# Kernel optimization log

Measured on AMD Instinct MI355X. Metric: run time of the kernel, lower is better.

The kernel has to match this reference:

```python
import jax, jax.numpy as jnp
import numpy as np

DIM = 512
HEADS = 8
EPS = 1e-3  # keras LayerNormalization default epsilon


def setup_inputs() -> dict:
    key = jax.random.key(0)
    ks = jax.random.split(key, 12)
    B, H, W, C = 8, 32, 32, DIM
    s = 0.02
    return {
        "x": jax.random.normal(ks[0], (B, H, W, C), jnp.float32),
        "ln_gamma": jnp.ones((C,), jnp.float32),
        "ln_beta": jnp.zeros((C,), jnp.float32),
        "qkv_d_w": jax.random.normal(ks[1], (C, 3 * C), jnp.float32) * s,
        "qkv_d_b": jnp.zeros((3 * C,), jnp.float32),
        "qkv_s_w": jax.random.normal(ks[2], (C, 3 * C), jnp.float32) * s,
        "qkv_s_b": jnp.zeros((3 * C,), jnp.float32),
        "proj_d_w": jax.random.normal(ks[3], (C, C), jnp.float32) * s,
        "proj_d_b": jnp.zeros((C,), jnp.float32),
        "proj_s_w": jax.random.normal(ks[4], (C, C), jnp.float32) * s,
        "proj_s_b": jnp.zeros((C,), jnp.float32),
        "fusion_weight": jnp.ones((2,), jnp.float32),
    }


def _split_heads(t, B, N):
    # [B, N, C] -> [B, heads, N, head_dim]
    return t.reshape(B, N, HEADS, -1).transpose(0, 2, 1, 3)


def _merge_heads(t, B, N, C):
    # [B, heads, N, head_dim] -> [B, N, C]
    return t.transpose(0, 2, 1, 3).reshape(B, N, C)


def reference(x, ln_gamma, ln_beta, qkv_d_w, qkv_d_b, qkv_s_w, qkv_s_b,
              proj_d_w, proj_d_b, proj_s_w, proj_s_b, fusion_weight):
    B, H, W, C = x.shape
    N = H * W
    scale = (C // HEADS) ** -0.5

    xf = x.reshape(B, N, C)
    mu = jnp.mean(xf, axis=-1, keepdims=True)
    var = jnp.var(xf, axis=-1, keepdims=True)
    xf = (xf - mu) * jax.lax.rsqrt(var + EPS) * ln_gamma + ln_beta

    # dense (softmax) branch
    qkv_d = xf @ qkv_d_w + qkv_d_b
    q_d, k_d, v_d = (
        _split_heads(t, B, N) for t in jnp.split(qkv_d, 3, axis=-1)
    )
    logits_d = jnp.einsum("bhnd,bhmd->bhnm", q_d, k_d) * scale
    out_d = jnp.einsum("bhnm,bhmd->bhnd", jax.nn.softmax(logits_d, axis=-1), v_d)
    out_d = _merge_heads(out_d, B, N, C) @ proj_d_w + proj_d_b

    # sparse (relu^2) branch
    qkv_s = xf @ qkv_s_w + qkv_s_b
    q_s, k_s, v_s = (
        _split_heads(t, B, N) for t in jnp.split(qkv_s, 3, axis=-1)
    )
    rq = jnp.square(jax.nn.relu(q_s))
    rk = jnp.square(jax.nn.relu(k_s))
    logits_s = jnp.einsum("bhnd,bhmd->bhnm", rq, rk) * scale
    out_s = jnp.einsum("bhnm,bhmd->bhnd", logits_s, v_s)
    out_s = _merge_heads(out_s, B, N, C) @ proj_s_w + proj_s_b

    alpha = jax.nn.softmax(fusion_weight)
    out = alpha[0] * out_s + alpha[1] * out_d
    return out.reshape(B, H, W, C)
```

## Files before the change

kernel.cpp:

```cpp
#include <hip/hip_runtime.h>
#include <math.h>

#define M_ROWS   8192
#define CDIM     512
#define QKV_N    1536
#define NTOK     1024
#define HEADS    8
#define HD       64
#define EPS      1e-3f
#define SCALE    0.125f
#define SCL2E    0.18033688011112042f

typedef __attribute__((ext_vector_type(8))) short short8;
typedef __attribute__((ext_vector_type(4))) float f32x4;
typedef unsigned short ushort_t;


__device__ __forceinline__ ushort_t f2bf(float f) {
    union { float f; unsigned int u; } v; v.f = f;
    unsigned int r = v.u + 0x7fffu + ((v.u >> 16) & 1u);
    return (ushort_t)(r >> 16);
}
__device__ __forceinline__ float bf2f(ushort_t u) {
    union { unsigned int u; float f; } v; v.u = ((unsigned int)u) << 16;
    return v.f;
}

__device__ __forceinline__ void get_alpha(const float* __restrict__ fw,
                                          float& a0, float& a1)
{
    const float m  = fmaxf(fw[0], fw[1]);
    const float e0 = __expf(fw[0] - m);
    const float e1 = __expf(fw[1] - m);
    const float inv = 1.0f / (e0 + e1);
    a0 = e0 * inv;
    a1 = e1 * inv;
}


__global__ __launch_bounds__(256) void ln_kernel(const float* __restrict__ x,
                                                 const float* __restrict__ gamma,
                                                 const float* __restrict__ beta,
                                                 ushort_t* __restrict__ xhi,
                                                 ushort_t* __restrict__ xlo)
{
    const int row = blockIdx.x;
    const int t   = threadIdx.x;
    const float2 v = ((const float2*)(x + (size_t)row * CDIM))[t];
    float s  = v.x + v.y;
    float ss = v.x * v.x + v.y * v.y;
#pragma unroll
    for (int off = 32; off > 0; off >>= 1) {
        s  += __shfl_xor(s,  off, 64);
        ss += __shfl_xor(ss, off, 64);
    }
    __shared__ float red[8];
    __shared__ float stats[2];
    const int wid = t >> 6, lane = t & 63;
    if (lane == 0) { red[wid] = s; red[4 + wid] = ss; }
    __syncthreads();
    if (t == 0) {
        const float S  = red[0] + red[1] + red[2] + red[3];
        const float SS = red[4] + red[5] + red[6] + red[7];
        const float mu  = S * (1.0f / CDIM);
        const float var = SS * (1.0f / CDIM) - mu * mu;
        stats[0] = mu;
        stats[1] = rsqrtf(var + EPS);
    }
    __syncthreads();
    const float mu = stats[0], rs = stats[1];
    const float2 gv = ((const float2*)gamma)[t];
    const float2 bv = ((const float2*)beta)[t];
    const float ox = (v.x - mu) * rs * gv.x + bv.x;
    const float oy = (v.y - mu) * rs * gv.y + bv.y;
    ushort2 h2, l2;
    h2.x = f2bf(ox); l2.x = f2bf(ox - bf2f(h2.x));
    h2.y = f2bf(oy); l2.y = f2bf(oy - bf2f(h2.y));
    ((ushort2*)(xhi + (size_t)row * CDIM))[t] = h2;
    ((ushort2*)(xlo + (size_t)row * CDIM))[t] = l2;
}


__global__ __launch_bounds__(256) void tconv_kernel(const float* __restrict__ W,
                                                    ushort_t* __restrict__ hiT,
                                                    ushort_t* __restrict__ loT,
                                                    int N, int ors, int coff)
{
    const int t  = threadIdx.x;
    const int bk = blockIdx.x * 64, bn = blockIdx.y * 64;
    __shared__ float tile[64][65];
#pragma unroll
    for (int i = 0; i < 4; ++i) {
        const int idx = t + i * 256;
        const int kl = idx >> 4, nl = (idx & 15) * 4;
        const float4 v = *(const float4*)(W + (size_t)(bk + kl) * N + bn + nl);
        tile[kl][nl] = v.x; tile[kl][nl + 1] = v.y;
        tile[kl][nl + 2] = v.z; tile[kl][nl + 3] = v.w;
    }
    __syncthreads();
#pragma unroll
    for (int i = 0; i < 2; ++i) {
        const int idx = t + i * 256;
        const int nl = idx >> 3, kc = (idx & 7) * 8;
        short8 hv, lv;
#pragma unroll
        for (int j = 0; j < 8; ++j) {
            const float f = tile[kc + j][nl];
            const ushort_t h = f2bf(f);
            hv[j] = (short)h;
            lv[j] = (short)f2bf(f - bf2f(h));
        }
        const size_t ob = (size_t)(bn + nl) * ors + coff + bk + kc;
        *(short8*)(hiT + ob) = hv;
        if (loT) *(short8*)(loT + ob) = lv;
    }
}


template<int SPLIT, int OUTBF>
__global__ __launch_bounds__(256) void gemm_bf16_mfma(const ushort_t* __restrict__ Ahi,
                                                      const ushort_t* __restrict__ Alo,
                                                      const ushort_t* __restrict__ Bhi,
                                                      const ushort_t* __restrict__ Blo,
                                                      const float* __restrict__ bias,
                                                      float* __restrict__ C,
                                                      ushort_t* __restrict__ Cb,
                                                      int N, int K)
{
    const int t  = threadIdx.x;
    const int l  = t & 63, w = t >> 6;
    const int wr = w >> 1, wc = w & 1;
    const int lr = l & 15, lg = l >> 4;
    const int bm = blockIdx.x * 128, bn = blockIdx.y * 128;

    __shared__ ushort_t As[SPLIT ? 2 : 1][128 * 64];
    __shared__ ushort_t Bs[SPLIT ? 2 : 1][128 * 64];

    f32x4 acc[4][4];
#pragma unroll
    for (int i = 0; i < 4; ++i)
#pragma unroll
        for (int j = 0; j < 4; ++j) acc[i][j] = (f32x4){0.f, 0.f, 0.f, 0.f};

    const int srow0  = t >> 3;
    const int schunk = t & 7;

    for (int kt = 0; kt < K; kt += 64) {
        __syncthreads();
#pragma unroll
        for (int i = 0; i < 4; ++i) {
            const int row = srow0 + i * 32;
            const int cs  = ((schunk ^ (row & 7)) * 8);
            const size_t ga = (size_t)(bm + row) * K + kt + schunk * 8;
            const size_t gb = (size_t)(bn + row) * K + kt + schunk * 8;
            *(short8*)(&As[0][row * 64 + cs]) = *(const short8*)(Ahi + ga);
            *(short8*)(&Bs[0][row * 64 + cs]) = *(const short8*)(Bhi + gb);
            if (SPLIT) {
                *(short8*)(&As[1][row * 64 + cs]) = *(const short8*)(Alo + ga);
                *(short8*)(&Bs[1][row * 64 + cs]) = *(const short8*)(Blo + gb);
            }
        }
        __syncthreads();
#pragma unroll
        for (int ks = 0; ks < 2; ++ks) {
            short8 ah[4], bh[4], al[4], bl[4];
#pragma unroll
            for (int mf = 0; mf < 4; ++mf) {
                const int row = wr * 64 + mf * 16 + lr;
                const int cs  = (((ks * 4 + lg) ^ (row & 7)) * 8);
                ah[mf] = *(const short8*)(&As[0][row * 64 + cs]);
                if (SPLIT) al[mf] = *(const short8*)(&As[1][row * 64 + cs]);
            }
#pragma unroll
            for (int nf = 0; nf < 4; ++nf) {
                const int row = wc * 64 + nf * 16 + lr;
                const int cs  = (((ks * 4 + lg) ^ (row & 7)) * 8);
                bh[nf] = *(const short8*)(&Bs[0][row * 64 + cs]);
                if (SPLIT) bl[nf] = *(const short8*)(&Bs[1][row * 64 + cs]);
            }
#pragma unroll
            for (int mf = 0; mf < 4; ++mf)
#pragma unroll
                for (int nf = 0; nf < 4; ++nf) {
                    acc[mf][nf] = __builtin_amdgcn_mfma_f32_16x16x32_bf16(ah[mf], bh[nf], acc[mf][nf], 0, 0, 0);
                    if (SPLIT) {
                        acc[mf][nf] = __builtin_amdgcn_mfma_f32_16x16x32_bf16(al[mf], bh[nf], acc[mf][nf], 0, 0, 0);
                        acc[mf][nf] = __builtin_amdgcn_mfma_f32_16x16x32_bf16(ah[mf], bl[nf], acc[mf][nf], 0, 0, 0);
                    }
                }
        }
    }
    float bv[4];
#pragma unroll
    for (int nf = 0; nf < 4; ++nf) bv[nf] = bias[bn + wc * 64 + nf * 16 + lr];
#pragma unroll
    for (int mf = 0; mf < 4; ++mf)
#pragma unroll
        for (int r = 0; r < 4; ++r) {
            const int row = bm + wr * 64 + mf * 16 + lg * 4 + r;
            if (OUTBF) {
                ushort_t* cp = Cb + (size_t)row * N + bn + wc * 64;
#pragma unroll
                for (int nf = 0; nf < 4; ++nf)
                    cp[nf * 16 + lr] = f2bf(acc[mf][nf][r] + bv[nf]);
            } else {
                float* cp = C + (size_t)row * N + bn + wc * 64;
#pragma unroll
                for (int nf = 0; nf < 4; ++nf)
                    cp[nf * 16 + lr] = acc[mf][nf][r] + bv[nf];
            }
        }
}


__global__ __launch_bounds__(256) void vt_kernel(const ushort_t* __restrict__ qkvd_bf,
                                                 ushort_t* __restrict__ vtg)
{
    const int t  = threadIdx.x;
    const int bh = blockIdx.x, nt = blockIdx.y;
    const int b  = bh >> 3, h = bh & 7;
    __shared__ ushort_t tile[64 * 72];
    const int row = t >> 2, c16 = (t & 3) * 16;
    const size_t src = (size_t)(b * NTOK + nt * 64 + row) * QKV_N + 2 * CDIM + h * HD + c16;
    *(short8*)(tile + row * 72 + c16)     = *(const short8*)(qkvd_bf + src);
    *(short8*)(tile + row * 72 + c16 + 8) = *(const short8*)(qkvd_bf + src + 8);
    __syncthreads();
    const int d = t >> 2, tc = (t & 3) * 16;
    short8 o0, o1;
#pragma unroll
    for (int i = 0; i < 8; ++i) {
        o0[i] = (short)tile[(tc + i) * 72 + d];
        o1[i] = (short)tile[(tc + 8 + i) * 72 + d];
    }
    const size_t dst = ((size_t)bh * 64 + d) * NTOK + nt * 64 + tc;
    *(short8*)(vtg + dst)     = o0;
    *(short8*)(vtg + dst + 8) = o1;
}


__global__ __launch_bounds__(256) void attn_dense_mfma(const ushort_t* __restrict__ qkvd_bf,
                                                       const ushort_t* __restrict__ vtg,
                                                       const float* __restrict__ fw,
                                                       ushort_t* __restrict__ athi,
                                                       ushort_t* __restrict__ atlo)
{
    const int t  = threadIdx.x;
    const int l  = t & 63;
    const int w  = t >> 6;
    const int lr = l & 15;
    const int lg = l >> 4;

    const int blk = blockIdx.x;
    const int xcd = blk & 7;
    const int ixl = blk >> 3;
    const int bh  = ((ixl >> 4) << 3) + xcd;
    const int qt  = ixl & 15;
    const int b   = bh >> 3, h = bh & 7;

    __shared__ ushort_t Qs[64 * 72];
    __shared__ ushort_t Ks[64 * 72];
    __shared__ ushort_t Vs[64 * 72];
    __shared__ ushort_t Pq[64 * 72];

    const int srow = t >> 2, sc = (t & 3) * 16;

    {
        const size_t src = (size_t)(b * NTOK + qt * 64 + srow) * QKV_N + h * HD + sc;
        *(short8*)(Qs + srow * 72 + sc)     = *(const short8*)(qkvd_bf + src);
        *(short8*)(Qs + srow * 72 + sc + 8) = *(const short8*)(qkvd_bf + src + 8);
    }
    __syncthreads();

    const short8 bQ0 = *(const short8*)(Qs + (w * 16 + lr) * 72 + lg * 8);
    const short8 bQ1 = *(const short8*)(Qs + (w * 16 + lr) * 72 + 32 + lg * 8);

    f32x4 oacc[4];
#pragma unroll
    for (int i = 0; i < 4; ++i) oacc[i] = (f32x4){0.f, 0.f, 0.f, 0.f};
    float lsum = 0.f;

    for (int kt2 = 0; kt2 < 16; ++kt2) {
        __syncthreads();
        {
            const size_t ksrc = (size_t)(b * NTOK + kt2 * 64 + srow) * QKV_N + CDIM + h * HD + sc;
            *(short8*)(Ks + srow * 72 + sc)     = *(const short8*)(qkvd_bf + ksrc);
            *(short8*)(Ks + srow * 72 + sc + 8) = *(const short8*)(qkvd_bf + ksrc + 8);
            const size_t vsrc = ((size_t)bh * 64 + srow) * NTOK + kt2 * 64 + sc;
            *(short8*)(Vs + srow * 72 + sc)     = *(const short8*)(vtg + vsrc);
            *(short8*)(Vs + srow * 72 + sc + 8) = *(const short8*)(vtg + vsrc + 8);
        }
        __syncthreads();

#pragma unroll
        for (int kb = 0; kb < 4; ++kb) {
            const short8 aK0 = *(const short8*)(Ks + (kb * 16 + lr) * 72 + lg * 8);
            const short8 aK1 = *(const short8*)(Ks + (kb * 16 + lr) * 72 + 32 + lg * 8);
            f32x4 z = {0.f, 0.f, 0.f, 0.f};
            z = __builtin_amdgcn_mfma_f32_16x16x32_bf16(aK0, bQ0, z, 0, 0, 0);
            z = __builtin_amdgcn_mfma_f32_16x16x32_bf16(aK1, bQ1, z, 0, 0, 0);
            const float p0 = exp2f(z[0] * SCL2E);
            const float p1 = exp2f(z[1] * SCL2E);
            const float p2 = exp2f(z[2] * SCL2E);
            const float p3 = exp2f(z[3] * SCL2E);
            lsum += (p0 + p1) + (p2 + p3);
            unsigned int r01, r23;
            asm("v_cvt_pk_bf16_f32 %0, %1, %2" : "=v"(r01) : "v"(p0), "v"(p1));
            asm("v_cvt_pk_bf16_f32 %0, %1, %2" : "=v"(r23) : "v"(p2), "v"(p3));
            uint2 pw; pw.x = r01; pw.y = r23;
            *(uint2*)(Pq + (w * 16 + lr) * 72 + kb * 16 + lg * 4) = pw;
        }

        const short8 bP0 = *(const short8*)(Pq + (w * 16 + lr) * 72 + lg * 8);
        const short8 bP1 = *(const short8*)(Pq + (w * 16 + lr) * 72 + 32 + lg * 8);
#pragma unroll
        for (int nfd = 0; nfd < 4; ++nfd) {
            const short8 aV0 = *(const short8*)(Vs + (nfd * 16 + lr) * 72 + lg * 8);
            const short8 aV1 = *(const short8*)(Vs + (nfd * 16 + lr) * 72 + 32 + lg * 8);
            oacc[nfd] = __builtin_amdgcn_mfma_f32_16x16x32_bf16(aV0, bP0, oacc[nfd], 0, 0, 0);
            oacc[nfd] = __builtin_amdgcn_mfma_f32_16x16x32_bf16(aV1, bP1, oacc[nfd], 0, 0, 0);
        }
    }

    lsum += __shfl_xor(lsum, 16, 64);
    lsum += __shfl_xor(lsum, 32, 64);
    float a0, a1;
    get_alpha(fw, a0, a1);
    const float sc2 = a1 / lsum;
    const size_t orow = ((size_t)(b * NTOK + qt * 64 + w * 16 + lr)) * 1024 + CDIM + h * HD;
#pragma unroll
    for (int nfd = 0; nfd < 4; ++nfd) {
        ushort4 hw, lw;
#pragma unroll
        for (int r = 0; r < 4; ++r) {
            const float v = oacc[nfd][r] * sc2;
            const ushort_t hv = f2bf(v);
            ((ushort_t*)&hw)[r] = hv;
            ((ushort_t*)&lw)[r] = f2bf(v - bf2f(hv));
        }
        *(ushort4*)(athi + orow + nfd * 16 + lg * 4) = hw;
        *(ushort4*)(atlo + orow + nfd * 16 + lg * 4) = lw;
    }
}


__global__ __launch_bounds__(256) void sparse_kv_kernel(const float* __restrict__ qkvs,
                                                        float* __restrict__ kvpart)
{
    const int t     = threadIdx.x;
    const int bh    = blockIdx.x >> 2;
    const int chunk = blockIdx.x & 3;
    const int b     = bh >> 3, h = bh & 7;
    const int j     = t >> 2, g = t & 3;
    __shared__ __align__(16) float ks[64 * 68];
    __shared__ __align__(16) float vs[64 * 68];
    float4 acc[4];
#pragma unroll
    for (int c4 = 0; c4 < 4; ++c4) acc[c4] = make_float4(0.f, 0.f, 0.f, 0.f);

    const size_t bbase = (size_t)b * NTOK * QKV_N;
    for (int mt = chunk * 4; mt < chunk * 4 + 4; ++mt) {
        __syncthreads();
        {
            const float* ksrc = qkvs + bbase + (size_t)(mt * 64) * QKV_N + CDIM + h * HD;
            const float* vsrc = ksrc + CDIM;
#pragma unroll
            for (int i = 0; i < 4; ++i) {
                const int idx = t + i * 256;
                const int row = idx >> 4, c4 = (idx & 15) * 4;
                *(float4*)(ks + row * 68 + c4) = *(const float4*)(ksrc + (size_t)row * QKV_N + c4);
                *(float4*)(vs + row * 68 + c4) = *(const float4*)(vsrc + (size_t)row * QKV_N + c4);
            }
        }
        __syncthreads();
#pragma unroll 4
        for (int m = 0; m < 64; ++m) {
            const float kkv = ks[m * 68 + j];
            const float rk  = fmaxf(kkv, 0.f);
            const float rk2 = rk * rk;
#pragma unroll
            for (int c4 = 0; c4 < 4; ++c4) {
                const float4 vv = *(const float4*)(vs + m * 68 + g * 16 + c4 * 4);
                acc[c4].x += rk2 * vv.x; acc[c4].y += rk2 * vv.y;
                acc[c4].z += rk2 * vv.z; acc[c4].w += rk2 * vv.w;
            }
        }
    }
#pragma unroll
    for (int c4 = 0; c4 < 4; ++c4) {
        float4 w = acc[c4];
        w.x *= SCALE; w.y *= SCALE; w.z *= SCALE; w.w *= SCALE;
        *(float4*)(kvpart + ((size_t)blockIdx.x << 12) + j * 64 + g * 16 + c4 * 4) = w;
    }
}


__global__ __launch_bounds__(256) void sparse_out_kernel(const float* __restrict__ qkvs,
                                                         const float* __restrict__ kvpart,
                                                         const float* __restrict__ fw,
                                                         ushort_t* __restrict__ athi,
                                                         ushort_t* __restrict__ atlo)
{
    const int t   = threadIdx.x;
    const int blk = blockIdx.x;
    const int qt  = blk & 15;
    const int bh  = blk >> 4;
    const int b   = bh >> 3, h = bh & 7;
    const int r   = t >> 2, g = t & 3;
    __shared__ __align__(16) float qs[64 * 68];
    __shared__ __align__(16) float kvs[64 * 68];
    {
        const float* qsrc = qkvs + (size_t)b * NTOK * QKV_N + (size_t)(qt * 64) * QKV_N + h * HD;
        const float* p0 = kvpart + ((size_t)(bh * 4) << 12);
#pragma unroll
        for (int i = 0; i < 4; ++i) {
            const int idx = t + i * 256;
            const int row = idx >> 4, c4 = (idx & 15) * 4;
            *(float4*)(qs + row * 68 + c4) = *(const float4*)(qsrc + (size_t)row * QKV_N + c4);
            const int o = row * 64 + c4;
            float4 s0 = *(const float4*)(p0 + o);
            const float4 s1 = *(const float4*)(p0 + 4096 + o);
            const float4 s2 = *(const float4*)(p0 + 8192 + o);
            const float4 s3 = *(const float4*)(p0 + 12288 + o);
            s0.x += s1.x + s2.x + s3.x; s0.y += s1.y + s2.y + s3.y;
            s0.z += s1.z + s2.z + s3.z; s0.w += s1.w + s2.w + s3.w;
            *(float4*)(kvs + row * 68 + c4) = s0;
        }
    }
    __syncthreads();
    float4 acc[4];
#pragma unroll
    for (int c4 = 0; c4 < 4; ++c4) acc[c4] = make_float4(0.f, 0.f, 0.f, 0.f);
#pragma unroll 4
    for (int jj = 0; jj < 64; ++jj) {
        const float qv  = qs[r * 68 + jj];
        const float rq  = fmaxf(qv, 0.f);
        const float rq2 = rq * rq;
#pragma unroll
        for (int c4 = 0; c4 < 4; ++c4) {
            const float4 kvv = *(const float4*)(kvs + jj * 68 + g * 16 + c4 * 4);
            acc[c4].x += rq2 * kvv.x; acc[c4].y += rq2 * kvv.y;
            acc[c4].z += rq2 * kvv.z; acc[c4].w += rq2 * kvv.w;
        }
    }
    float a0, a1;
    get_alpha(fw, a0, a1);
    const size_t orow = ((size_t)(b * NTOK + qt * 64 + r)) * 1024 + h * HD;
#pragma unroll
    for (int c4 = 0; c4 < 4; ++c4) {
        float4 w = acc[c4];
        w.x *= a0; w.y *= a0; w.z *= a0; w.w *= a0;
        ushort4 hw, lw;
        hw.x = f2bf(w.x); lw.x = f2bf(w.x - bf2f(hw.x));
        hw.y = f2bf(w.y); lw.y = f2bf(w.y - bf2f(hw.y));
        hw.z = f2bf(w.z); lw.z = f2bf(w.z - bf2f(hw.z));
        hw.w = f2bf(w.w); lw.w = f2bf(w.w - bf2f(hw.w));
        *(ushort4*)(athi + orow + g * 16 + c4 * 4) = hw;
        *(ushort4*)(atlo + orow + g * 16 + c4 * 4) = lw;
    }
}


__global__ void bias_comb_kernel(const float* __restrict__ bs,
                                 const float* __restrict__ bd,
                                 const float* __restrict__ fw,
                                 float* __restrict__ out)
{
    float a0, a1;
    get_alpha(fw, a0, a1);
    const int t = threadIdx.x;
    out[t] = a0 * bs[t] + a1 * bd[t];
}


extern "C" void kernel_launch(void* const* d_in, const int* in_sizes, int n_in,
                              void* d_out, int out_size, void* d_ws, size_t ws_size,
                              hipStream_t stream)
{
    (void)in_sizes; (void)n_in; (void)out_size; (void)ws_size;

    const float* x        = (const float*)d_in[0];
    const float* ln_g     = (const float*)d_in[1];
    const float* ln_b     = (const float*)d_in[2];
    const float* qkv_d_w  = (const float*)d_in[3];
    const float* qkv_d_b  = (const float*)d_in[4];
    const float* qkv_s_w  = (const float*)d_in[5];
    const float* qkv_s_b  = (const float*)d_in[6];
    const float* proj_d_w = (const float*)d_in[7];
    const float* proj_d_b = (const float*)d_in[8];
    const float* proj_s_w = (const float*)d_in[9];
    const float* proj_s_b = (const float*)d_in[10];
    const float* fw       = (const float*)d_in[11];

    float* ws = (float*)d_ws;
    float*    qkvs    = ws;
    float*    kvpart  = ws + (size_t)12582912;
    float*    biasc   = ws + (size_t)13631488;
    ushort_t* qkvd_bf = (ushort_t*)(ws + (size_t)14680064);
    ushort_t* vtg     = (ushort_t*)(ws + (size_t)20971520);
    ushort_t* athi    = (ushort_t*)(ws + (size_t)23068672);
    ushort_t* atlo    = (ushort_t*)(ws + (size_t)27262976);
    ushort_t* xhi     = (ushort_t*)(ws + (size_t)31457280);
    ushort_t* xlo     = (ushort_t*)(ws + (size_t)33554432);
    ushort_t* WdT_hi  = (ushort_t*)(ws + (size_t)35651584);
    ushort_t* WsT_hi  = (ushort_t*)(ws + (size_t)36044800);
    ushort_t* WsT_lo  = (ushort_t*)(ws + (size_t)36438016);
    ushort_t* WpT_hi  = (ushort_t*)(ws + (size_t)36831232);
    ushort_t* WpT_lo  = (ushort_t*)(ws + (size_t)37093376);

    ln_kernel<<<8192, 256, 0, stream>>>(x, ln_g, ln_b, xhi, xlo);
    tconv_kernel<<<dim3(8, 24), 256, 0, stream>>>(qkv_d_w, WdT_hi, nullptr, QKV_N, CDIM, 0);
    tconv_kernel<<<dim3(8, 24), 256, 0, stream>>>(qkv_s_w, WsT_hi, WsT_lo, QKV_N, CDIM, 0);
    tconv_kernel<<<dim3(8, 8), 256, 0, stream>>>(proj_s_w, WpT_hi, WpT_lo, CDIM, 1024, 0);
    tconv_kernel<<<dim3(8, 8), 256, 0, stream>>>(proj_d_w, WpT_hi, WpT_lo, CDIM, 1024, 512);
    bias_comb_kernel<<<1, 512, 0, stream>>>(proj_s_b, proj_d_b, fw, biasc);

    gemm_bf16_mfma<0, 1><<<dim3(64, 12), 256, 0, stream>>>(xhi, nullptr, WdT_hi, nullptr,
                                                           qkv_d_b, nullptr, qkvd_bf, QKV_N, CDIM);
    gemm_bf16_mfma<1, 0><<<dim3(64, 12), 256, 0, stream>>>(xhi, xlo, WsT_hi, WsT_lo,
                                                           qkv_s_b, qkvs, nullptr, QKV_N, CDIM);

    vt_kernel<<<dim3(64, 16), 256, 0, stream>>>(qkvd_bf, vtg);
    attn_dense_mfma<<<1024, 256, 0, stream>>>(qkvd_bf, vtg, fw, athi, atlo);

    sparse_kv_kernel<<<256, 256, 0, stream>>>(qkvs, kvpart);
    sparse_out_kernel<<<1024, 256, 0, stream>>>(qkvs, kvpart, fw, athi, atlo);

    gemm_bf16_mfma<1, 0><<<dim3(64, 4), 256, 0, stream>>>(athi, atlo, WpT_hi, WpT_lo,
                                                          biasc, (float*)d_out, nullptr, CDIM, 1024);
}
```

Baseline: 210.7 us.

## Fuse dense and sparse QKV GEMMs; drop low-part split for dense projection half

```diff
diff --git a/kernel.cpp b/kernel.cpp
--- a/kernel.cpp
+++ b/kernel.cpp
@@ -117,7 +117,7 @@
 }
 
 
-template<int SPLIT, int OUTBF>
+template<int MODE, int OUTBF>
 __global__ __launch_bounds__(256) void gemm_bf16_mfma(const ushort_t* __restrict__ Ahi,
                                                       const ushort_t* __restrict__ Alo,
                                                       const ushort_t* __restrict__ Bhi,
@@ -125,7 +125,7 @@
                                                       const float* __restrict__ bias,
                                                       float* __restrict__ C,
                                                       ushort_t* __restrict__ Cb,
-                                                      int N, int K)
+                                                      int N, int K, int KS)
 {
     const int t  = threadIdx.x;
     const int l  = t & 63, w = t >> 6;
@@ -133,8 +133,8 @@
     const int lr = l & 15, lg = l >> 4;
     const int bm = blockIdx.x * 128, bn = blockIdx.y * 128;
 
-    __shared__ ushort_t As[SPLIT ? 2 : 1][128 * 64];
-    __shared__ ushort_t Bs[SPLIT ? 2 : 1][128 * 64];
+    __shared__ ushort_t As[MODE ? 2 : 1][128 * 64];
+    __shared__ ushort_t Bs[MODE ? 2 : 1][128 * 64];
 
     f32x4 acc[4][4];
 #pragma unroll
@@ -146,6 +146,7 @@
     const int schunk = t & 7;
 
     for (int kt = 0; kt < K; kt += 64) {
+        const bool lo = MODE && (MODE == 1 || kt < KS);
         __syncthreads();
 #pragma unroll
         for (int i = 0; i < 4; ++i) {
@@ -155,9 +156,9 @@
             const size_t gb = (size_t)(bn + row) * K + kt + schunk * 8;
             *(short8*)(&As[0][row * 64 + cs]) = *(const short8*)(Ahi + ga);
             *(short8*)(&Bs[0][row * 64 + cs]) = *(const short8*)(Bhi + gb);
-            if (SPLIT) {
-                *(short8*)(&As[1][row * 64 + cs]) = *(const short8*)(Alo + ga);
-                *(short8*)(&Bs[1][row * 64 + cs]) = *(const short8*)(Blo + gb);
+            if (lo) {
+                *(short8*)(&As[MODE ? 1 : 0][row * 64 + cs]) = *(const short8*)(Alo + ga);
+                *(short8*)(&Bs[MODE ? 1 : 0][row * 64 + cs]) = *(const short8*)(Blo + gb);
             }
         }
         __syncthreads();
@@ -169,21 +170,21 @@
                 const int row = wr * 64 + mf * 16 + lr;
                 const int cs  = (((ks * 4 + lg) ^ (row & 7)) * 8);
                 ah[mf] = *(const short8*)(&As[0][row * 64 + cs]);
-                if (SPLIT) al[mf] = *(const short8*)(&As[1][row * 64 + cs]);
+                if (lo) al[mf] = *(const short8*)(&As[MODE ? 1 : 0][row * 64 + cs]);
             }
 #pragma unroll
             for (int nf = 0; nf < 4; ++nf) {
                 const int row = wc * 64 + nf * 16 + lr;
                 const int cs  = (((ks * 4 + lg) ^ (row & 7)) * 8);
                 bh[nf] = *(const short8*)(&Bs[0][row * 64 + cs]);
-                if (SPLIT) bl[nf] = *(const short8*)(&Bs[1][row * 64 + cs]);
+                if (lo) bl[nf] = *(const short8*)(&Bs[MODE ? 1 : 0][row * 64 + cs]);
             }
 #pragma unroll
             for (int mf = 0; mf < 4; ++mf)
 #pragma unroll
                 for (int nf = 0; nf < 4; ++nf) {
                     acc[mf][nf] = __builtin_amdgcn_mfma_f32_16x16x32_bf16(ah[mf], bh[nf], acc[mf][nf], 0, 0, 0);
-                    if (SPLIT) {
+                    if (lo) {
                         acc[mf][nf] = __builtin_amdgcn_mfma_f32_16x16x32_bf16(al[mf], bh[nf], acc[mf][nf], 0, 0, 0);
                         acc[mf][nf] = __builtin_amdgcn_mfma_f32_16x16x32_bf16(ah[mf], bl[nf], acc[mf][nf], 0, 0, 0);
                     }
@@ -208,6 +209,104 @@
 #pragma unroll
                 for (int nf = 0; nf < 4; ++nf)
                     cp[nf * 16 + lr] = acc[mf][nf][r] + bv[nf];
+            }
+        }
+}
+
+
+__global__ __launch_bounds__(256) void gemm_qkv_fused(const ushort_t* __restrict__ Ahi,
+                                                      const ushort_t* __restrict__ Alo,
+                                                      const ushort_t* __restrict__ Bdhi,
+                                                      const ushort_t* __restrict__ Bshi,
+                                                      const ushort_t* __restrict__ Bslo,
+                                                      const float* __restrict__ bias_d,
+                                                      const float* __restrict__ bias_s,
+                                                      ushort_t* __restrict__ Cd,
+                                                      float* __restrict__ Cs,
+                                                      int N, int K)
+{
+    const int t  = threadIdx.x;
+    const int l  = t & 63, w = t >> 6;
+    const int wr = w >> 1, wc = w & 1;
+    const int lr = l & 15, lg = l >> 4;
+    const int bm = blockIdx.x * 128, bn = blockIdx.y * 128;
+
+    __shared__ ushort_t As[2][128 * 64];
+    __shared__ ushort_t Bs[3][128 * 64];
+
+    f32x4 accd[4][4], accs[4][4];
+#pragma unroll
+    for (int i = 0; i < 4; ++i)
+#pragma unroll
+        for (int j = 0; j < 4; ++j) {
+            accd[i][j] = (f32x4){0.f, 0.f, 0.f, 0.f};
+            accs[i][j] = (f32x4){0.f, 0.f, 0.f, 0.f};
+        }
+
+    const int srow0  = t >> 3;
+    const int schunk = t & 7;
+
+    for (int kt = 0; kt < K; kt += 64) {
+        __syncthreads();
+#pragma unroll
+        for (int i = 0; i < 4; ++i) {
+            const int row = srow0 + i * 32;
+            const int cs  = ((schunk ^ (row & 7)) * 8);
+            const size_t ga = (size_t)(bm + row) * K + kt + schunk * 8;
+            const size_t gb = (size_t)(bn + row) * K + kt + schunk * 8;
+            *(short8*)(&As[0][row * 64 + cs]) = *(const short8*)(Ahi + ga);
+            *(short8*)(&As[1][row * 64 + cs]) = *(const short8*)(Alo + ga);
+            *(short8*)(&Bs[0][row * 64 + cs]) = *(const short8*)(Bdhi + gb);
+            *(short8*)(&Bs[1][row * 64 + cs]) = *(const short8*)(Bshi + gb);
+            *(short8*)(&Bs[2][row * 64 + cs]) = *(const short8*)(Bslo + gb);
+        }
+        __syncthreads();
+#pragma unroll
+        for (int ks = 0; ks < 2; ++ks) {
+            short8 ah[4], al[4], bd[4], bsh[4], bsl[4];
+#pragma unroll
+            for (int mf = 0; mf < 4; ++mf) {
+                const int row = wr * 64 + mf * 16 + lr;
+                const int cs  = (((ks * 4 + lg) ^ (row & 7)) * 8);
+                ah[mf] = *(const short8*)(&As[0][row * 64 + cs]);
+                al[mf] = *(const short8*)(&As[1][row * 64 + cs]);
+            }
+#pragma unroll
+            for (int nf = 0; nf < 4; ++nf) {
+                const int row = wc * 64 + nf * 16 + lr;
+                const int cs  = (((ks * 4 + lg) ^ (row & 7)) * 8);
+                bd[nf]  = *(const short8*)(&Bs[0][row * 64 + cs]);
+                bsh[nf] = *(const short8*)(&Bs[1][row * 64 + cs]);
+                bsl[nf] = *(const short8*)(&Bs[2][row * 64 + cs]);
+            }
+#pragma unroll
+            for (int mf = 0; mf < 4; ++mf)
+#pragma unroll
+                for (int nf = 0; nf < 4; ++nf) {
+                    accd[mf][nf] = __builtin_amdgcn_mfma_f32_16x16x32_bf16(ah[mf], bd[nf],  accd[mf][nf], 0, 0, 0);
+                    accs[mf][nf] = __builtin_amdgcn_mfma_f32_16x16x32_bf16(ah[mf], bsh[nf], accs[mf][nf], 0, 0, 0);
+                    accs[mf][nf] = __builtin_amdgcn_mfma_f32_16x16x32_bf16(al[mf], bsh[nf], accs[mf][nf], 0, 0, 0);
+                    accs[mf][nf] = __builtin_amdgcn_mfma_f32_16x16x32_bf16(ah[mf], bsl[nf], accs[mf][nf], 0, 0, 0);
+                }
+        }
+    }
+    float bvd[4], bvs[4];
+#pragma unroll
+    for (int nf = 0; nf < 4; ++nf) {
+        bvd[nf] = bias_d[bn + wc * 64 + nf * 16 + lr];
+        bvs[nf] = bias_s[bn + wc * 64 + nf * 16 + lr];
+    }
+#pragma unroll
+    for (int mf = 0; mf < 4; ++mf)
+#pragma unroll
+        for (int r = 0; r < 4; ++r) {
+            const int row = bm + wr * 64 + mf * 16 + lg * 4 + r;
+            ushort_t* cpd = Cd + (size_t)row * N + bn + wc * 64;
+            float*    cps = Cs + (size_t)row * N + bn + wc * 64;
+#pragma unroll
+            for (int nf = 0; nf < 4; ++nf) {
+                cpd[nf * 16 + lr] = f2bf(accd[mf][nf][r] + bvd[nf]);
+                cps[nf * 16 + lr] = accs[mf][nf][r] + bvs[nf];
             }
         }
 }
@@ -241,8 +340,7 @@
 __global__ __launch_bounds__(256) void attn_dense_mfma(const ushort_t* __restrict__ qkvd_bf,
                                                        const ushort_t* __restrict__ vtg,
                                                        const float* __restrict__ fw,
-                                                       ushort_t* __restrict__ athi,
-                                                       ushort_t* __restrict__ atlo)
+                                                       ushort_t* __restrict__ athi)
 {
     const int t  = threadIdx.x;
     const int l  = t & 63;
@@ -329,16 +427,11 @@
     const size_t orow = ((size_t)(b * NTOK + qt * 64 + w * 16 + lr)) * 1024 + CDIM + h * HD;
 #pragma unroll
     for (int nfd = 0; nfd < 4; ++nfd) {
-        ushort4 hw, lw;
-#pragma unroll
-        for (int r = 0; r < 4; ++r) {
-            const float v = oacc[nfd][r] * sc2;
-            const ushort_t hv = f2bf(v);
-            ((ushort_t*)&hw)[r] = hv;
-            ((ushort_t*)&lw)[r] = f2bf(v - bf2f(hv));
-        }
+        ushort4 hw;
+#pragma unroll
+        for (int r = 0; r < 4; ++r)
+            ((ushort_t*)&hw)[r] = f2bf(oacc[nfd][r] * sc2);
         *(ushort4*)(athi + orow + nfd * 16 + lg * 4) = hw;
-        *(ushort4*)(atlo + orow + nfd * 16 + lg * 4) = lw;
     }
 }
 
@@ -511,20 +604,20 @@
     tconv_kernel<<<dim3(8, 24), 256, 0, stream>>>(qkv_d_w, WdT_hi, nullptr, QKV_N, CDIM, 0);
     tconv_kernel<<<dim3(8, 24), 256, 0, stream>>>(qkv_s_w, WsT_hi, WsT_lo, QKV_N, CDIM, 0);
     tconv_kernel<<<dim3(8, 8), 256, 0, stream>>>(proj_s_w, WpT_hi, WpT_lo, CDIM, 1024, 0);
-    tconv_kernel<<<dim3(8, 8), 256, 0, stream>>>(proj_d_w, WpT_hi, WpT_lo, CDIM, 1024, 512);
+    tconv_kernel<<<dim3(8, 8), 256, 0, stream>>>(proj_d_w, WpT_hi, nullptr, CDIM, 1024, 512);
     bias_comb_kernel<<<1, 512, 0, stream>>>(proj_s_b, proj_d_b, fw, biasc);
 
-    gemm_bf16_mfma<0, 1><<<dim3(64, 12), 256, 0, stream>>>(xhi, nullptr, WdT_hi, nullptr,
-                                                           qkv_d_b, nullptr, qkvd_bf, QKV_N, CDIM);
-    gemm_bf16_mfma<1, 0><<<dim3(64, 12), 256, 0, stream>>>(xhi, xlo, WsT_hi, WsT_lo,
-                                                           qkv_s_b, qkvs, nullptr, QKV_N, CDIM);
+    gemm_qkv_fused<<<dim3(64, 12), 256, 0, stream>>>(xhi, xlo, WdT_hi, WsT_hi, WsT_lo,
+                                                     qkv_d_b, qkv_s_b, qkvd_bf, qkvs,
+                                                     QKV_N, CDIM);
 
     vt_kernel<<<dim3(64, 16), 256, 0, stream>>>(qkvd_bf, vtg);
-    attn_dense_mfma<<<1024, 256, 0, stream>>>(qkvd_bf, vtg, fw, athi, atlo);
+    attn_dense_mfma<<<1024, 256, 0, stream>>>(qkvd_bf, vtg, fw, athi);
 
     sparse_kv_kernel<<<256, 256, 0, stream>>>(qkvs, kvpart);
     sparse_out_kernel<<<1024, 256, 0, stream>>>(qkvs, kvpart, fw, athi, atlo);
 
-    gemm_bf16_mfma<1, 0><<<dim3(64, 4), 256, 0, stream>>>(athi, atlo, WpT_hi, WpT_lo,
-                                                          biasc, (float*)d_out, nullptr, CDIM, 1024);
-}
+    gemm_bf16_mfma<2, 0><<<dim3(64, 4), 256, 0, stream>>>(athi, atlo, WpT_hi, WpT_lo,
+                                                          biasc, (float*)d_out, nullptr,
+                                                          CDIM, 1024, 512);
+}
```

Measured after the change: 222.3 us. 1.05x slower.
